# Kernel optimization log

Measured on AMD Instinct MI355X. Metric: run time of the kernel, lower is better.

Reference implementation:

```python
import jax, jax.numpy as jnp
import numpy as np

B, C, H, W = 8, 256, 64, 64
CQK = C // 8  # 32


def setup_inputs() -> dict:
    key = jax.random.key(0)
    ks = jax.random.split(key, 7)
    s = 0.02
    return {
        "feat_map": jax.random.normal(ks[0], (B, C, H, W), dtype=jnp.float32),
        "w1": jax.random.normal(ks[1], (CQK, C), dtype=jnp.float32) * s,
        "b1": jnp.zeros((CQK,), dtype=jnp.float32),
        "w2": jax.random.normal(ks[2], (CQK, C), dtype=jnp.float32) * s,
        "b2": jnp.zeros((CQK,), dtype=jnp.float32),
        "w3": jax.random.normal(ks[3], (C, C), dtype=jnp.float32) * s,
        "b3": jnp.zeros((C,), dtype=jnp.float32),
        "gamma": jnp.zeros((1,), dtype=jnp.float32),
    }


def reference(feat_map, w1, b1, w2, b2, w3, b3, gamma):
    b, c, h, w = feat_map.shape
    n = h * w
    x = feat_map.reshape(b, c, n)  # [B, C, N]
    # 1x1 convs == per-pixel linear maps over channels
    q = jnp.einsum("oc,bcn->bno", w1, x) + b1  # [B, N, C//8]
    k = jnp.einsum("oc,bcn->bon", w2, x) + b2[None, :, None]  # [B, C//8, N]
    v = jnp.einsum("oc,bcn->bon", w3, x) + b3[None, :, None]  # [B, C, N]
    relation = jnp.einsum("bno,bom->bnm", q, k)  # [B, N, N]
    attn = jax.nn.softmax(relation, axis=-1)  # softmax over last dim
    # feat_refine = bmm(v, attn^T): out[:, :, i] = sum_j v[:, :, j] * attn[i, j]
    feat_refine = jnp.einsum("bcm,bnm->bcn", v, attn).reshape(b, c, h, w)
    scaled = gamma[0] * feat_refine
    return (feat_refine, scaled)
```

## Files before the change

kernel.cpp:

```cpp
#include <hip/hip_runtime.h>
#include <cmath>

#define NB 8
#define CC 256
#define NPIX 4096
#define QB 128
#define KVB 64
#define NT2 32
#define LOG2E 1.4426950408889634f

typedef __attribute__((ext_vector_type(4))) float f32x4;
typedef __attribute__((ext_vector_type(16))) float f32x16;
typedef __attribute__((ext_vector_type(8))) short s16x8;
typedef __attribute__((ext_vector_type(4))) unsigned int u32x4;
typedef __attribute__((ext_vector_type(2))) unsigned int u32x2;

__device__ __forceinline__ unsigned short f2bf(float f) {
    union { float f; unsigned int u; } v; v.f = f;
    return (unsigned short)((v.u + 0x7FFFu + ((v.u >> 16) & 1u)) >> 16);
}

__device__ __forceinline__ unsigned int cvt_pk_bf16(float lo, float hi) {
    unsigned int r;
    asm("v_cvt_pk_bf16_f32 %0, %1, %2" : "=v"(r) : "v"(lo), "v"(hi));
    return r;
}

__device__ __forceinline__ float u2f(unsigned int u) {
    union { unsigned int u; float f; } v; v.u = u; return v.f;
}

__global__ __launch_bounds__(320) void proj_gemm_kernel(
    const float* __restrict__ x,
    const float* __restrict__ w1, const float* __restrict__ b1,
    const float* __restrict__ w2, const float* __restrict__ b2,
    const float* __restrict__ w3, const float* __restrict__ b3,
    unsigned short* __restrict__ Qm, unsigned short* __restrict__ Km,
    unsigned short* __restrict__ Vm)
{
    const int b  = blockIdx.x >> 6;
    const int n0 = (blockIdx.x & 63) * 64;
    const int wave = threadIdx.x >> 6;
    const int lane = threadIdx.x & 63;
    const int cl = lane & 15, g = lane >> 4;

    const float* arow[4];
#pragma unroll
    for (int ct = 0; ct < 4; ++ct) {
        const int row = wave * 64 + ct * 16 + cl;
        if (row < 32)       arow[ct] = w1 + (size_t)row * 256;
        else if (row < 64)  arow[ct] = w2 + (size_t)(row - 32) * 256;
        else                arow[ct] = w3 + (size_t)(row - 64) * 256;
    }

    const float* xb = x + (size_t)b * CC * NPIX + n0 + cl;

    f32x4 acc[4][4];
#pragma unroll
    for (int ct = 0; ct < 4; ++ct)
#pragma unroll
        for (int nt = 0; nt < 4; ++nt) acc[ct][nt] = (f32x4){0.f, 0.f, 0.f, 0.f};

    for (int ks = 0; ks < 8; ++ks) {
        const int c0 = ks * 32;
        s16x8 ah[4];
#pragma unroll
        for (int ct = 0; ct < 4; ++ct) {
            const float* ap = arow[ct] + c0 + g * 8;
            f32x4 a0 = *(const f32x4*)ap;
            f32x4 a1 = *(const f32x4*)(ap + 4);
            u32x4 u;
            u[0] = cvt_pk_bf16(a0[0], a0[1]); u[1] = cvt_pk_bf16(a0[2], a0[3]);
            u[2] = cvt_pk_bf16(a1[0], a1[1]); u[3] = cvt_pk_bf16(a1[2], a1[3]);
            ah[ct] = __builtin_bit_cast(s16x8, u);
        }
#pragma unroll
        for (int nt = 0; nt < 4; ++nt) {
            const float* xp = xb + (size_t)(c0 + g * 8) * NPIX + nt * 16;
            float xe[8];
#pragma unroll
            for (int e = 0; e < 8; ++e) xe[e] = xp[(size_t)e * NPIX];
            u32x4 uh, ul;
#pragma unroll
            for (int p = 0; p < 4; ++p) {
                const unsigned int hp = cvt_pk_bf16(xe[2 * p], xe[2 * p + 1]);
                const float h0 = u2f(hp << 16);
                const float h1 = u2f(hp & 0xffff0000u);
                uh[p] = hp;
                ul[p] = cvt_pk_bf16(xe[2 * p] - h0, xe[2 * p + 1] - h1);
            }
            const s16x8 bh = __builtin_bit_cast(s16x8, uh);
            const s16x8 bl = __builtin_bit_cast(s16x8, ul);
#pragma unroll
            for (int ct = 0; ct < 4; ++ct)
                acc[ct][nt] = __builtin_amdgcn_mfma_f32_16x16x32_bf16(ah[ct], bh, acc[ct][nt], 0, 0, 0);
#pragma unroll
            for (int ct = 0; ct < 4; ++ct)
                acc[ct][nt] = __builtin_amdgcn_mfma_f32_16x16x32_bf16(ah[ct], bl, acc[ct][nt], 0, 0, 0);
        }
    }

    if (wave == 0) {
#pragma unroll
        for (int ct = 0; ct < 4; ++ct) {
#pragma unroll
            for (int nt = 0; nt < 4; ++nt) {
                const int n = n0 + nt * 16 + cl;
                const int co = ct * 16 + g * 4;
                f32x4 v = acc[ct][nt];
                if (ct < 2) {
                    const float q0 = (v[0] + b1[co + 0]) * LOG2E;
                    const float q1 = (v[1] + b1[co + 1]) * LOG2E;
                    const float q2 = (v[2] + b1[co + 2]) * LOG2E;
                    const float q3 = (v[3] + b1[co + 3]) * LOG2E;
                    u32x2 dd = {cvt_pk_bf16(q0, q1), cvt_pk_bf16(q2, q3)};
                    *(u32x2*)(Qm + ((size_t)b * NPIX + n) * 32 + co) = dd;
                } else {
                    const int ko = co - 32;
                    const float k0 = v[0] + b2[ko + 0];
                    const float k1 = v[1] + b2[ko + 1];
                    const float k2 = v[2] + b2[ko + 2];
                    const float k3 = v[3] + b2[ko + 3];
                    u32x2 dd = {cvt_pk_bf16(k0, k1), cvt_pk_bf16(k2, k3)};
                    *(u32x2*)(Km + ((size_t)b * NPIX + n) * 32 + ko) = dd;
                }
            }
        }
    } else {
        const int cvb = (wave - 1) * 64;
#pragma unroll
        for (int ct = 0; ct < 4; ++ct) {
#pragma unroll
            for (int nt = 0; nt < 4; ++nt) {
                const int n = n0 + nt * 16 + cl;
                const int cv = cvb + ct * 16 + g * 4;
#pragma unroll
                for (int r = 0; r < 4; ++r)
                    Vm[((size_t)b * CC + cv + r) * NPIX + n] = f2bf(acc[ct][nt][r] + b3[cv + r]);
            }
        }
    }
}

__global__ __launch_bounds__(512, 2) void attn_kernel(
    const unsigned short* __restrict__ Qm, const unsigned short* __restrict__ Km,
    const unsigned short* __restrict__ Vm, const float* __restrict__ gamma,
    float* __restrict__ out)
{
    __shared__ unsigned short Vs[2][2][CC * KVB];
    __shared__ float mArr[2][4][32];
    __shared__ float lArr[2][4][32];

    const int bid = ((blockIdx.x & 7) << 5) + (blockIdx.x >> 3);
    const int b = bid >> 5;
    const int q0 = (bid & 31) * QB;

    const int t = threadIdx.x;
    const int wave = t >> 6;
    const int lane = t & 63;
    const int q_ = lane & 31;
    const int hi = lane >> 5;
    const int s = wave & 3;
    const int h = wave >> 2;

    const int qrow = q0 + s * 32 + q_;

    s16x8 qf[2];
#pragma unroll
    for (int kh = 0; kh < 2; ++kh)
        qf[kh] = *(const s16x8*)(Qm + ((size_t)b * NPIX + qrow) * 32 + kh * 16 + hi * 8);

    f32x16 acc[8];
#pragma unroll
    for (int ct = 0; ct < 8; ++ct) acc[ct] = (f32x16){};

    float mrun = -__builtin_inff();
    float lrun = 0.f;

    const unsigned short* Kg = Km + (size_t)b * NPIX * 32;
    const unsigned short* Vg = Vm + (size_t)b * CC * NPIX;

    const int tg = t & 255;
    const int vr0 = tg >> 3;
    const int cg = (tg & 7) ^ (vr0 & 7);
    const unsigned short* vsrc = Vg + (size_t)vr0 * NPIX + cg * 8;

#define STAGE_V(tile, buf_)                                                    \
    {                                                                          \
        const int mm_ = h * 2048 + (tile) * KVB;                               \
        _Pragma("unroll")                                                      \
        for (int i_ = 0; i_ < 8; ++i_)                                         \
            __builtin_amdgcn_global_load_lds(                                  \
                (const __attribute__((address_space(1))) void*)(vsrc + (size_t)i_ * 32 * NPIX + mm_), \
                (__attribute__((address_space(3))) void*)(&Vs[h][buf_][i_ * 2048 + tg * 8]), \
                16, 0, 0);                                                     \
    }

    s16x8 kf[2][2];
#define LOAD_KF(mm_)                                                           \
    {                                                                          \
        _Pragma("unroll")                                                      \
        for (int mt_ = 0; mt_ < 2; ++mt_)                                      \
            _Pragma("unroll")                                                  \
            for (int kh_ = 0; kh_ < 2; ++kh_)                                  \
                kf[mt_][kh_] = *(const s16x8*)(Kg + (size_t)((mm_) + 32 * mt_ + q_) * 32 + kh_ * 16 + hi * 8); \
    }

#define QK_TILE()                                                              \
    {                                                                          \
        f32x16 z_ = (f32x16){};                                                \
        s0 = __builtin_amdgcn_mfma_f32_32x32x16_bf16(kf[0][0], qf[0], z_, 0, 0, 0); \
        s0 = __builtin_amdgcn_mfma_f32_32x32x16_bf16(kf[0][1], qf[1], s0, 0, 0, 0); \
        s1 = __builtin_amdgcn_mfma_f32_32x32x16_bf16(kf[1][0], qf[0], z_, 0, 0, 0); \
        s1 = __builtin_amdgcn_mfma_f32_32x32x16_bf16(kf[1][1], qf[1], s1, 0, 0, 0); \
    }

#define SOFTMAX_PACK(PW_)                                                      \
    {                                                                          \
        float tm_[16];                                                         \
        _Pragma("unroll")                                                      \
        for (int i_ = 0; i_ < 16; ++i_) tm_[i_] = fmaxf(s0[i_], s1[i_]);       \
        _Pragma("unroll")                                                      \
        for (int i_ = 0; i_ < 8; ++i_) tm_[i_] = fmaxf(tm_[i_], tm_[i_ + 8]);  \
        _Pragma("unroll")                                                      \
        for (int i_ = 0; i_ < 4; ++i_) tm_[i_] = fmaxf(tm_[i_], tm_[i_ + 4]);  \
        const float ml_ = fmaxf(fmaxf(tm_[0], tm_[1]), fmaxf(tm_[2], tm_[3])); \
        if (!__all(ml_ <= mrun + 8.f)) {                                       \
            float mw_ = fmaxf(ml_, __shfl_xor(ml_, 32, 64));                   \
            const float mnew_ = fmaxf(mrun, mw_);                              \
            const float alpha_ = __builtin_amdgcn_exp2f(mrun - mnew_);         \
            mrun = mnew_;                                                      \
            lrun *= alpha_;                                                    \
            _Pragma("unroll")                                                  \
            for (int ct_ = 0; ct_ < 8; ++ct_) acc[ct_] *= alpha_;              \
        }                                                                      \
        _Pragma("unroll")                                                      \
        for (int r_ = 0; r_ < 16; ++r_) {                                      \
            s0[r_] = __builtin_amdgcn_exp2f(s0[r_] - mrun);                    \
            s1[r_] = __builtin_amdgcn_exp2f(s1[r_] - mrun);                    \
        }                                                                      \
        float ts_[16];                                                         \
        _Pragma("unroll")                                                      \
        for (int i_ = 0; i_ < 16; ++i_) ts_[i_] = s0[i_] + s1[i_];             \
        _Pragma("unroll")                                                      \
        for (int i_ = 0; i_ < 8; ++i_) ts_[i_] += ts_[i_ + 8];                 \
        _Pragma("unroll")                                                      \
        for (int i_ = 0; i_ < 4; ++i_) ts_[i_] += ts_[i_ + 4];                 \
        lrun += (ts_[0] + ts_[1]) + (ts_[2] + ts_[3]);                         \
        unsigned int w0_[4][2], w1_[4][2];                                     \
        _Pragma("unroll")                                                      \
        for (int p_ = 0; p_ < 4; ++p_) {                                       \
            w0_[p_][0] = cvt_pk_bf16(s0[4 * p_ + 0], s0[4 * p_ + 1]);          \
            w0_[p_][1] = cvt_pk_bf16(s0[4 * p_ + 2], s0[4 * p_ + 3]);          \
            w1_[p_][0] = cvt_pk_bf16(s1[4 * p_ + 0], s1[4 * p_ + 1]);          \
            w1_[p_][1] = cvt_pk_bf16(s1[4 * p_ + 2], s1[4 * p_ + 3]);          \
        }                                                                      \
        _Pragma("unroll")                                                      \
        for (int t4_ = 0; t4_ < 4; ++t4_) {                                    \
            const int lt_ = t4_ & 1;                                           \
            unsigned int a0_ = (t4_ < 2) ? w0_[2 * lt_][0] : w1_[2 * lt_][0];  \
            unsigned int b0_ = (t4_ < 2) ? w0_[2 * lt_ + 1][0] : w1_[2 * lt_ + 1][0]; \
            unsigned int a1_ = (t4_ < 2) ? w0_[2 * lt_][1] : w1_[2 * lt_][1];  \
            unsigned int b1_ = (t4_ < 2) ? w0_[2 * lt_ + 1][1] : w1_[2 * lt_ + 1][1]; \
            asm("v_permlane32_swap_b32 %0, %1" : "+v"(a0_), "+v"(b0_));        \
            asm("v_permlane32_swap_b32 %0, %1" : "+v"(a1_), "+v"(b1_));        \
            PW_[t4_] = (u32x4){a0_, a1_, b0_, b1_};                            \
        }                                                                      \
    }

#define PV_TILE(bufsel_, PW_)                                                  \
    {                                                                          \
        __builtin_amdgcn_s_setprio(1);                                         \
        _Pragma("unroll")                                                      \
        for (int t4_ = 0; t4_ < 4; ++t4_) {                                    \
            const s16x8 pb_ = __builtin_bit_cast(s16x8, PW_[t4_]);             \
            _Pragma("unroll")                                                  \
            for (int ct_ = 0; ct_ < 8; ++ct_) {                                \
                const int c_ = 32 * ct_ + q_;                                  \
                const int slot_ = (2 * t4_ + hi) ^ (c_ & 7);                   \
                const s16x8 av_ = *(const s16x8*)(&Vs[h][bufsel_][c_ * 64 + slot_ * 8]); \
                acc[ct_] = __builtin_amdgcn_mfma_f32_32x32x16_bf16(av_, pb_, acc[ct_], 0, 0, 0); \
            }                                                                  \
        }                                                                      \
        __builtin_amdgcn_s_setprio(0);                                         \
    }

    f32x16 s0, s1;
    u32x4 pw[4];
    if (h == 0) {
        STAGE_V(0, 0)
        LOAD_KF(0)
    }

    int cur = 0;
    for (int it = 0; it < NT2; ++it) {
        __syncthreads();

        if (h == 0) {
            if (it < NT2 - 1) STAGE_V(it + 1, cur ^ 1)
            QK_TILE()
            LOAD_KF((((it + 1) & (NT2 - 1))) * KVB)
            SOFTMAX_PACK(pw)
            PV_TILE(cur, pw)
        } else {
            STAGE_V(it, cur)
            LOAD_KF(2048 + it * KVB)
            if (it > 0) PV_TILE(cur ^ 1, pw)
            QK_TILE()
            SOFTMAX_PACK(pw)
        }

        cur ^= 1;
    }

    __syncthreads();

    if (h == 1) PV_TILE((NT2 - 1) & 1, pw)

    lrun += __shfl_xor(lrun, 32, 64);

    if (lane < 32) { mArr[h][s][lane] = mrun; lArr[h][s][lane] = lrun; }
    __syncthreads();

    const float m_o = mArr[h ^ 1][s][q_];
    const float l_o = lArr[h ^ 1][s][q_];
    const float M = fmaxf(mrun, m_o);
    const float f = __builtin_amdgcn_exp2f(mrun - M);
    const float l_tot = lrun * f + l_o * __builtin_amdgcn_exp2f(m_o - M);

    float* S = (float*)&Vs[0][0][0];
    if (h == 1) {
#pragma unroll
        for (int ct = 0; ct < 8; ++ct)
#pragma unroll
            for (int r = 0; r < 16; ++r)
                S[(ct * 16 + r) * 256 + s * 64 + lane] = acc[ct][r] * f;
    }
    __syncthreads();

    if (h == 0) {
        const float inv = 1.f / l_tot;
        const float gm = gamma[0];
        float* out2 = out + (size_t)NB * CC * NPIX;
        const int n = qrow;
#pragma unroll
        for (int ct = 0; ct < 8; ++ct) {
#pragma unroll
            for (int r = 0; r < 16; ++r) {
                const int c = 32 * ct + (r & 3) + 8 * (r >> 2) + 4 * hi;
                const float val = (acc[ct][r] * f + S[(ct * 16 + r) * 256 + s * 64 + lane]) * inv;
                const size_t idx = ((size_t)b * CC + c) * NPIX + n;
                out[idx] = val;
                out2[idx] = gm * val;
            }
        }
    }
}

extern "C" void kernel_launch(void* const* d_in, const int* in_sizes, int n_in,
                              void* d_out, int out_size, void* d_ws, size_t ws_size,
                              hipStream_t stream) {
    (void)in_sizes; (void)n_in; (void)out_size; (void)ws_size;
    const float* x     = (const float*)d_in[0];
    const float* w1    = (const float*)d_in[1];
    const float* b1    = (const float*)d_in[2];
    const float* w2    = (const float*)d_in[3];
    const float* b2    = (const float*)d_in[4];
    const float* w3    = (const float*)d_in[5];
    const float* b3    = (const float*)d_in[6];
    const float* gamma = (const float*)d_in[7];
    float* out = (float*)d_out;

    unsigned short* Qm = (unsigned short*)d_ws;
    unsigned short* Km = Qm + (size_t)NB * NPIX * 32;
    unsigned short* Vm = Km + (size_t)NB * NPIX * 32;

    proj_gemm_kernel<<<NB * 64, 320, 0, stream>>>(x, w1, b1, w2, b2, w3, b3, Qm, Km, Vm);
    attn_kernel<<<NB * 32, 512, 0, stream>>>(Qm, Km, Vm, gamma, out);
}
```

Baseline: 132.6 us.

## Unify both wave halves into a software-pipelined window with delayed PV

Replaces the asymmetric schedule, where one wave half ran PV right after softmax and the other lagged by one tile, with a single symmetric pipeline for both halves. Each step now stages V, computes QK and the softmax, then issues the PV MMA for the previous tile. Two ping-pong P register sets let the loop unroll by two without register copies. The accumulator rescale is moved after the delayed PV so the previous tile's contribution is also scaled, at the cost of holding an extra P buffer in registers.

```diff
diff --git a/kernel.cpp b/kernel.cpp
--- a/kernel.cpp
+++ b/kernel.cpp
@@ -215,59 +215,6 @@
         s1 = __builtin_amdgcn_mfma_f32_32x32x16_bf16(kf[1][1], qf[1], s1, 0, 0, 0); \
     }
 
-#define SOFTMAX_PACK(PW_)                                                      \
-    {                                                                          \
-        float tm_[16];                                                         \
-        _Pragma("unroll")                                                      \
-        for (int i_ = 0; i_ < 16; ++i_) tm_[i_] = fmaxf(s0[i_], s1[i_]);       \
-        _Pragma("unroll")                                                      \
-        for (int i_ = 0; i_ < 8; ++i_) tm_[i_] = fmaxf(tm_[i_], tm_[i_ + 8]);  \
-        _Pragma("unroll")                                                      \
-        for (int i_ = 0; i_ < 4; ++i_) tm_[i_] = fmaxf(tm_[i_], tm_[i_ + 4]);  \
-        const float ml_ = fmaxf(fmaxf(tm_[0], tm_[1]), fmaxf(tm_[2], tm_[3])); \
-        if (!__all(ml_ <= mrun + 8.f)) {                                       \
-            float mw_ = fmaxf(ml_, __shfl_xor(ml_, 32, 64));                   \
-            const float mnew_ = fmaxf(mrun, mw_);                              \
-            const float alpha_ = __builtin_amdgcn_exp2f(mrun - mnew_);         \
-            mrun = mnew_;                                                      \
-            lrun *= alpha_;                                                    \
-            _Pragma("unroll")                                                  \
-            for (int ct_ = 0; ct_ < 8; ++ct_) acc[ct_] *= alpha_;              \
-        }                                                                      \
-        _Pragma("unroll")                                                      \
-        for (int r_ = 0; r_ < 16; ++r_) {                                      \
-            s0[r_] = __builtin_amdgcn_exp2f(s0[r_] - mrun);                    \
-            s1[r_] = __builtin_amdgcn_exp2f(s1[r_] - mrun);                    \
-        }                                                                      \
-        float ts_[16];                                                         \
-        _Pragma("unroll")                                                      \
-        for (int i_ = 0; i_ < 16; ++i_) ts_[i_] = s0[i_] + s1[i_];             \
-        _Pragma("unroll")                                                      \
-        for (int i_ = 0; i_ < 8; ++i_) ts_[i_] += ts_[i_ + 8];                 \
-        _Pragma("unroll")                                                      \
-        for (int i_ = 0; i_ < 4; ++i_) ts_[i_] += ts_[i_ + 4];                 \
-        lrun += (ts_[0] + ts_[1]) + (ts_[2] + ts_[3]);                         \
-        unsigned int w0_[4][2], w1_[4][2];                                     \
-        _Pragma("unroll")                                                      \
-        for (int p_ = 0; p_ < 4; ++p_) {                                       \
-            w0_[p_][0] = cvt_pk_bf16(s0[4 * p_ + 0], s0[4 * p_ + 1]);          \
-            w0_[p_][1] = cvt_pk_bf16(s0[4 * p_ + 2], s0[4 * p_ + 3]);          \
-            w1_[p_][0] = cvt_pk_bf16(s1[4 * p_ + 0], s1[4 * p_ + 1]);          \
-            w1_[p_][1] = cvt_pk_bf16(s1[4 * p_ + 2], s1[4 * p_ + 3]);          \
-        }                                                                      \
-        _Pragma("unroll")                                                      \
-        for (int t4_ = 0; t4_ < 4; ++t4_) {                                    \
-            const int lt_ = t4_ & 1;                                           \
-            unsigned int a0_ = (t4_ < 2) ? w0_[2 * lt_][0] : w1_[2 * lt_][0];  \
-            unsigned int b0_ = (t4_ < 2) ? w0_[2 * lt_ + 1][0] : w1_[2 * lt_ + 1][0]; \
-            unsigned int a1_ = (t4_ < 2) ? w0_[2 * lt_][1] : w1_[2 * lt_][1];  \
-            unsigned int b1_ = (t4_ < 2) ? w0_[2 * lt_ + 1][1] : w1_[2 * lt_ + 1][1]; \
-            asm("v_permlane32_swap_b32 %0, %1" : "+v"(a0_), "+v"(b0_));        \
-            asm("v_permlane32_swap_b32 %0, %1" : "+v"(a1_), "+v"(b1_));        \
-            PW_[t4_] = (u32x4){a0_, a1_, b0_, b1_};                            \
-        }                                                                      \
-    }
-
 #define PV_TILE(bufsel_, PW_)                                                  \
     {                                                                          \
         __builtin_amdgcn_s_setprio(1);                                         \
@@ -285,37 +232,79 @@
         __builtin_amdgcn_s_setprio(0);                                         \
     }
 
+#define WINDOW(IT, PWOLD, PWNEW, DOPV)                                         \
+    {                                                                          \
+        __syncthreads();   \
+        STAGE_V(IT, (IT) & 1)                                                  \
+        QK_TILE()                                                              \
+        float tm_[16];                                                         \
+        _Pragma("unroll")                                                      \
+        for (int i_ = 0; i_ < 16; ++i_) tm_[i_] = fmaxf(s0[i_], s1[i_]);       \
+        _Pragma("unroll")                                                      \
+        for (int i_ = 0; i_ < 8; ++i_) tm_[i_] = fmaxf(tm_[i_], tm_[i_ + 8]);  \
+        _Pragma("unroll")                                                      \
+        for (int i_ = 0; i_ < 4; ++i_) tm_[i_] = fmaxf(tm_[i_], tm_[i_ + 4]);  \
+        const float ml_ = fmaxf(fmaxf(tm_[0], tm_[1]), fmaxf(tm_[2], tm_[3])); \
+        const bool resc_ = !__all(ml_ <= mrun + 8.f);                          \
+        float alpha_ = 1.f;                                                    \
+        if (resc_) {       \
+            float mw_ = fmaxf(ml_, __shfl_xor(ml_, 32, 64));                   \
+            const float mnew_ = fmaxf(mrun, mw_);                              \
+            alpha_ = __builtin_amdgcn_exp2f(mrun - mnew_);                     \
+            mrun = mnew_;                                                      \
+            lrun *= alpha_;                                                    \
+        }                                                                      \
+        _Pragma("unroll")                                                      \
+        for (int r_ = 0; r_ < 16; ++r_) {                                      \
+            s0[r_] = __builtin_amdgcn_exp2f(s0[r_] - mrun);                    \
+            s1[r_] = __builtin_amdgcn_exp2f(s1[r_] - mrun);                    \
+        }                                                                      \
+        float ts_[16];                                                         \
+        _Pragma("unroll")                                                      \
+        for (int i_ = 0; i_ < 16; ++i_) ts_[i_] = s0[i_] + s1[i_];             \
+        _Pragma("unroll")                                                      \
+        for (int i_ = 0; i_ < 8; ++i_) ts_[i_] += ts_[i_ + 8];                 \
+        _Pragma("unroll")                                                      \
+        for (int i_ = 0; i_ < 4; ++i_) ts_[i_] += ts_[i_ + 4];                 \
+        lrun += (ts_[0] + ts_[1]) + (ts_[2] + ts_[3]);                         \
+        unsigned int w0_[4][2], w1_[4][2];                                     \
+        _Pragma("unroll")                                                      \
+        for (int p_ = 0; p_ < 4; ++p_) {                                       \
+            w0_[p_][0] = cvt_pk_bf16(s0[4 * p_ + 0], s0[4 * p_ + 1]);          \
+            w0_[p_][1] = cvt_pk_bf16(s0[4 * p_ + 2], s0[4 * p_ + 3]);          \
+            w1_[p_][0] = cvt_pk_bf16(s1[4 * p_ + 0], s1[4 * p_ + 1]);          \
+            w1_[p_][1] = cvt_pk_bf16(s1[4 * p_ + 2], s1[4 * p_ + 3]);          \
+        }                                                                      \
+        _Pragma("unroll")                                                      \
+        for (int t4_ = 0; t4_ < 4; ++t4_) {                                    \
+            const int lt_ = t4_ & 1;                                           \
+            unsigned int a0_ = (t4_ < 2) ? w0_[2 * lt_][0] : w1_[2 * lt_][0];  \
+            unsigned int b0_ = (t4_ < 2) ? w0_[2 * lt_ + 1][0] : w1_[2 * lt_ + 1][0]; \
+            unsigned int a1_ = (t4_ < 2) ? w0_[2 * lt_][1] : w1_[2 * lt_][1];  \
+            unsigned int b1_ = (t4_ < 2) ? w0_[2 * lt_ + 1][1] : w1_[2 * lt_ + 1][1]; \
+            asm("v_permlane32_swap_b32 %0, %1" : "+v"(a0_), "+v"(b0_));        \
+            asm("v_permlane32_swap_b32 %0, %1" : "+v"(a1_), "+v"(b1_));        \
+            PWNEW[t4_] = (u32x4){a0_, a1_, b0_, b1_};                          \
+        }                                                                      \
+        LOAD_KF(h * 2048 + (((IT) + 1) & (NT2 - 1)) * KVB)                     \
+        if (DOPV) PV_TILE(((IT) + 1) & 1, PWOLD)                               \
+        if (resc_) {                                                           \
+            _Pragma("unroll")                                                  \
+            for (int ct_ = 0; ct_ < 8; ++ct_) acc[ct_] *= alpha_;              \
+        }                                                                      \
+    }
+
     f32x16 s0, s1;
-    u32x4 pw[4];
-    if (h == 0) {
-        STAGE_V(0, 0)
-        LOAD_KF(0)
-    }
-
-    int cur = 0;
-    for (int it = 0; it < NT2; ++it) {
-        __syncthreads();
-
-        if (h == 0) {
-            if (it < NT2 - 1) STAGE_V(it + 1, cur ^ 1)
-            QK_TILE()
-            LOAD_KF((((it + 1) & (NT2 - 1))) * KVB)
-            SOFTMAX_PACK(pw)
-            PV_TILE(cur, pw)
-        } else {
-            STAGE_V(it, cur)
-            LOAD_KF(2048 + it * KVB)
-            if (it > 0) PV_TILE(cur ^ 1, pw)
-            QK_TILE()
-            SOFTMAX_PACK(pw)
-        }
-
-        cur ^= 1;
+    u32x4 pwA[4], pwB[4];
+    LOAD_KF(h * 2048)
+
+    for (int it2 = 0; it2 < NT2; it2 += 2) {
+        WINDOW(it2, pwB, pwA, (it2 > 0))
+        WINDOW(it2 + 1, pwA, pwB, true)
     }
 
     __syncthreads();
-
-    if (h == 1) PV_TILE((NT2 - 1) & 1, pw)
+    PV_TILE(1, pwB)
 
     lrun += __shfl_xor(lrun, 32, 64);
 
```

Result: faster. 127.1 us (-4.2%).
